# Optimization experiments

Hardware: AMD Instinct MI355X
Metric: run time of the kernel (lower is better)

## Reference

```python
import jax, jax.numpy as jnp
import numpy as np

HIDDEN = 2048
HEADS = 16
HEAD_DIM = HIDDEN // HEADS          # 128
HALF = HEAD_DIM // 2                # 64
LATENT = HIDDEN // 4                # 512 (compression_ratio=4)
ROPE_BASE = 10000.0


def _rope_cos_sin(seq_len):
    # LlamaRotaryEmbedding with dim=HALF
    inv_freq = 1.0 / (ROPE_BASE ** (jnp.arange(0, HALF, 2, dtype=jnp.float32) / HALF))
    t = jnp.arange(seq_len, dtype=jnp.float32)
    freqs = jnp.einsum('i,j->ij', t, inv_freq)          # [S, HALF/2]
    emb = jnp.concatenate([freqs, freqs], axis=-1)       # [S, HALF]
    cos = jnp.cos(emb)[None, :, None, :]                 # [1,S,1,HALF]
    sin = jnp.sin(emb)[None, :, None, :]
    return cos, sin


def _rotate_half(x):
    x1, x2 = jnp.split(x, 2, axis=-1)
    return jnp.concatenate([-x2, x1], axis=-1)


def _apply_rope(x, cos, sin):
    return x * cos + _rotate_half(x) * sin


def setup_inputs() -> dict:
    key = jax.random.key(0)
    ks = jax.random.split(key, 10)
    B, S = 2, 2048
    std = 0.02
    inp = {
        'x':        jax.random.normal(ks[0], (B, S, HIDDEN), jnp.float32),
        # weights stored as [in, out] (transposed torch Linear weight)
        'W_kv_d':   jax.random.normal(ks[1], (HIDDEN, LATENT), jnp.float32) * std,
        'W_q_d':    jax.random.normal(ks[2], (HIDDEN, LATENT), jnp.float32) * std,
        'W_k_u':    jax.random.normal(ks[3], (LATENT, HEADS * HALF), jnp.float32) * std,
        'W_q_u':    jax.random.normal(ks[4], (LATENT, HEADS * HALF), jnp.float32) * std,
        'W_v_u':    jax.random.normal(ks[5], (LATENT, HIDDEN), jnp.float32) * std,
        'W_rope_k': jax.random.normal(ks[6], (HIDDEN, HIDDEN // 2), jnp.float32) * std,
        'W_rope_q': jax.random.normal(ks[7], (LATENT, HIDDEN // 2), jnp.float32) * std,
        'W_o':      jax.random.normal(ks[8], (HIDDEN, HIDDEN), jnp.float32) * std,
    }
    return inp


def reference(x, W_kv_d, W_q_d, W_k_u, W_q_u, W_v_u, W_rope_k, W_rope_q, W_o):
    B, S, _ = x.shape
    kv_latent = x @ W_kv_d                      # [B,S,LATENT]
    q_latent = x @ W_q_d                        # [B,S,LATENT]

    k = (kv_latent @ W_k_u).reshape(B, S, HEADS, HALF)
    q = (q_latent @ W_q_u).reshape(B, S, HEADS, HALF)
    v = (kv_latent @ W_v_u).reshape(B, S, HEADS, HEAD_DIM)

    q_rope = (q_latent @ W_rope_q).reshape(B, S, HEADS, HALF)
    k_rope = (x @ W_rope_k).reshape(B, S, HEADS, HALF)

    cos, sin = _rope_cos_sin(S)
    k_rope = _apply_rope(k_rope, cos, sin)
    q_rope = _apply_rope(q_rope, cos, sin)

    q = jnp.concatenate([q, q_rope], axis=-1)   # [B,S,H,HEAD_DIM]
    k = jnp.concatenate([k, k_rope], axis=-1)

    scale = 1.0 / jnp.sqrt(jnp.float32(HEAD_DIM))
    scores = jnp.einsum('bqhd,bkhd->bhqk', q, k) * scale   # [B,H,S,S]
    causal = jnp.tril(jnp.ones((S, S), dtype=bool))
    scores = jnp.where(causal[None, None], scores, jnp.float32(-1e30))
    attn = jax.nn.softmax(scores, axis=-1)
    y = jnp.einsum('bhqk,bkhd->bqhd', attn, v).reshape(B, S, HIDDEN)
    return y @ W_o
```

## Files before the change

### kernel.cpp

```cpp
#include <hip/hip_runtime.h>
#include <hip/hip_bf16.h>

typedef __hip_bfloat16 bf16;
typedef __attribute__((ext_vector_type(8))) short short8;
typedef __attribute__((ext_vector_type(4))) float f32x4;

#define AS1 __attribute__((address_space(1)))
#define AS3 __attribute__((address_space(3)))

__device__ __forceinline__ void gload_lds16(const bf16* gp, bf16* lp) {
  __builtin_amdgcn_global_load_lds((const AS1 void*)gp, (AS3 void*)lp, 16, 0, 0);
}

__device__ __forceinline__ float fast_exp2(float x) {
#if __has_builtin(__builtin_amdgcn_exp2f)
  return __builtin_amdgcn_exp2f(x);
#else
  return exp2f(x);
#endif
}

__device__ __forceinline__ void store_c(bf16* C, size_t idx, float v) { C[idx] = __float2bfloat16(v); }
__device__ __forceinline__ void store_c(float* C, size_t idx, float v) { C[idx] = v; }

struct __align__(8) b16x4 { bf16 a, b, c, d; };

__global__ void cvt_f32_bf16(const float* __restrict__ in, bf16* __restrict__ out) {
  const int i = (blockIdx.x * 256 + threadIdx.x) * 4;
  const float4 v = *(const float4*)(in + i);
  out[i + 0] = __float2bfloat16(v.x);
  out[i + 1] = __float2bfloat16(v.y);
  out[i + 2] = __float2bfloat16(v.z);
  out[i + 3] = __float2bfloat16(v.w);
}

__global__ void rope_tab_kernel(float2* __restrict__ ctab) {
  const int idx = blockIdx.x * 256 + threadIdx.x;
  const int i = idx & 31;
  const int s = idx >> 5;
  const float inv = fast_exp2(-(float)i * 0.41524101186092029f);
  const float ang = (float)s * inv;
  ctab[idx] = make_float2(cosf(ang), sinf(ang));
}

struct PrepArgs {
  const float* src[8];
  bf16* dst[8];
  int R[8], C[8], cum[8];
};

__global__ void prep_kernel(PrepArgs a) {
  __shared__ bf16 t[32][33];
  const int blk = blockIdx.x;
  int e = 0;
  while (e < 7 && blk >= a.cum[e]) ++e;
  const int lt = blk - (e ? a.cum[e - 1] : 0);
  const int R = a.R[e], C = a.C[e];
  const int tpr = C >> 5;
  const int bx = lt % tpr, by = lt / tpr;
  const float* in = a.src[e];
  bf16* out = a.dst[e];
  const int c0 = bx * 32, r0 = by * 32;
  const int tx = threadIdx.x, ty = threadIdx.y;
  for (int i = 0; i < 4; ++i)
    t[ty + 8 * i][tx] = __float2bfloat16(in[(size_t)(r0 + ty + 8 * i) * C + c0 + tx]);
  __syncthreads();
  for (int i = 0; i < 4; ++i)
    out[(size_t)(c0 + ty + 8 * i) * R + r0 + tx] = t[tx][ty + 8 * i];
}

template <typename CT, int MODE>
__global__ void gemm_bt(const bf16* __restrict__ A, int lda,
                        const bf16* __restrict__ Bt,
                        CT* __restrict__ C, bf16* __restrict__ C2, int ldc,
                        int K, const float2* __restrict__ ctab)
{
  __shared__ __align__(16) bf16 As[2][128 * 32];
  __shared__ __align__(16) bf16 Bs[2][128 * 32];
  const int tid  = threadIdx.x;
  const int wave = tid >> 6, lane = tid & 63;
  const int quad = lane >> 4, l16 = lane & 15;
  const int m0 = blockIdx.y * 128, n0 = blockIdx.x * 128;
  const int wm = (wave >> 1) * 64, wn = (wave & 1) * 64;

  f32x4 acc[4][4];
#pragma unroll
  for (int i = 0; i < 4; ++i)
#pragma unroll
    for (int j = 0; j < 4; ++j) acc[i][j] = (f32x4){0.f, 0.f, 0.f, 0.f};

  const int r1  = tid >> 2;
  const int ks1 = (tid & 3) * 8;

  gload_lds16(A  + (size_t)(m0 + r1)      * lda + ks1, &As[0][tid * 8]);
  gload_lds16(A  + (size_t)(m0 + r1 + 64) * lda + ks1, &As[0][(tid + 256) * 8]);
  gload_lds16(Bt + (size_t)(n0 + r1)      * K   + ks1, &Bs[0][tid * 8]);
  gload_lds16(Bt + (size_t)(n0 + r1 + 64) * K   + ks1, &Bs[0][(tid + 256) * 8]);

  int cur = 0;
  for (int k0 = 0; k0 < K; k0 += 32) {
    if (k0 + 32 < K) {
      const int kn = k0 + 32;
      const int nxt = cur ^ 1;
      gload_lds16(A  + (size_t)(m0 + r1)      * lda + kn + ks1, &As[nxt][tid * 8]);
      gload_lds16(A  + (size_t)(m0 + r1 + 64) * lda + kn + ks1, &As[nxt][(tid + 256) * 8]);
      gload_lds16(Bt + (size_t)(n0 + r1)      * K   + kn + ks1, &Bs[nxt][tid * 8]);
      gload_lds16(Bt + (size_t)(n0 + r1 + 64) * K   + kn + ks1, &Bs[nxt][(tid + 256) * 8]);
      asm volatile("s_waitcnt vmcnt(4)" ::: "memory");
    } else {
      asm volatile("s_waitcnt vmcnt(0)" ::: "memory");
    }
    __builtin_amdgcn_s_barrier();

    short8 af[4], bf_[4];
#pragma unroll
    for (int mt = 0; mt < 4; ++mt)
      af[mt] = *(const short8*)&As[cur][(wm + mt * 16 + l16) * 32 + quad * 8];
#pragma unroll
    for (int nt = 0; nt < 4; ++nt)
      bf_[nt] = *(const short8*)&Bs[cur][(wn + nt * 16 + l16) * 32 + quad * 8];
#pragma unroll
    for (int mt = 0; mt < 4; ++mt)
#pragma unroll
      for (int nt = 0; nt < 4; ++nt)
        acc[mt][nt] = __builtin_amdgcn_mfma_f32_16x16x32_bf16(af[mt], bf_[nt], acc[mt][nt], 0, 0, 0);
    __builtin_amdgcn_s_barrier();
    cur ^= 1;
  }

  if (MODE == 0) {
#pragma unroll
    for (int mt = 0; mt < 4; ++mt) {
      const int row = m0 + wm + mt * 16 + quad * 4;
#pragma unroll
      for (int nt = 0; nt < 4; ++nt) {
        const int cn = n0 + wn + nt * 16 + l16;
        const f32x4 v = acc[mt][nt];
#pragma unroll
        for (int r = 0; r < 4; ++r)
          store_c(C, (size_t)(row + r) * ldc + cn, v[r]);
      }
    }
  } else if (MODE == 4) {
    if (n0 < 1024) {
#pragma unroll
      for (int mt = 0; mt < 4; ++mt) {
        const int row = m0 + wm + mt * 16 + quad * 4;
#pragma unroll
        for (int nt = 0; nt < 4; ++nt) {
          const int cn = n0 + wn + nt * 16 + l16;
          const f32x4 v = acc[mt][nt];
#pragma unroll
          for (int r = 0; r < 4; ++r)
            store_c(C, (size_t)(row + r) * 1024 + cn, v[r]);
        }
      }
    } else {
#pragma unroll
      for (int mt = 0; mt < 4; ++mt) {
        const int row = m0 + wm + mt * 16 + quad * 4;
        f32x4 w[4];
#pragma unroll
        for (int nt = 0; nt < 4; ++nt) w[nt] = acc[mt][nt];
#pragma unroll
        for (int r = 0; r < 4; ++r) {
          const int s = (row + r) & 2047;
          const float2 cs0 = ctab[(s << 5) + l16];
          const float2 cs1 = ctab[(s << 5) + 16 + l16];
          const float x1a = w[0][r], x2a = w[2][r];
          const float x1b = w[1][r], x2b = w[3][r];
          w[0][r] = x1a * cs0.x - x2a * cs0.y;
          w[2][r] = x2a * cs0.x + x1a * cs0.y;
          w[1][r] = x1b * cs1.x - x2b * cs1.y;
          w[3][r] = x2b * cs1.x + x1b * cs1.y;
        }
#pragma unroll
        for (int nt = 0; nt < 4; ++nt) {
          const int cn2 = n0 + wn + nt * 16 + l16 - 1024;
          const int g = ((cn2 >> 6) << 7) + 64 + (cn2 & 63);
#pragma unroll
          for (int r = 0; r < 4; ++r)
            C2[(size_t)(row + r) * 2048 + g] = __float2bfloat16(w[nt][r]);
        }
      }
    }
  }
}

__global__ void gemm_up_fused(const bf16* __restrict__ latcat,
                              const bf16* __restrict__ wtUP,
                              const bf16* __restrict__ wtQcat,
                              bf16* __restrict__ vT, bf16* __restrict__ kfull,
                              bf16* __restrict__ qfull,
                              const float2* __restrict__ ctab)
{
  const bool is2 = (blockIdx.x >= 24);
  const bf16* A  = latcat + (is2 ? 512 : 0);
  const bf16* Bt = is2 ? wtQcat : wtUP;
  const int n0 = (is2 ? (int)blockIdx.x - 24 : (int)blockIdx.x) * 128;
  const int K = 512, lda = 1024;

  __shared__ __align__(16) bf16 As[2][128 * 32];
  __shared__ __align__(16) bf16 Bs[2][128 * 32];
  const int tid  = threadIdx.x;
  const int wave = tid >> 6, lane = tid & 63;
  const int quad = lane >> 4, l16 = lane & 15;
  const int m0 = blockIdx.y * 128;
  const int wm = (wave >> 1) * 64, wn = (wave & 1) * 64;

  f32x4 acc[4][4];
#pragma unroll
  for (int i = 0; i < 4; ++i)
#pragma unroll
    for (int j = 0; j < 4; ++j) acc[i][j] = (f32x4){0.f, 0.f, 0.f, 0.f};

  const int r1  = tid >> 2;
  const int ks1 = (tid & 3) * 8;

  gload_lds16(A  + (size_t)(m0 + r1)      * lda + ks1, &As[0][tid * 8]);
  gload_lds16(A  + (size_t)(m0 + r1 + 64) * lda + ks1, &As[0][(tid + 256) * 8]);
  gload_lds16(Bt + (size_t)(n0 + r1)      * K   + ks1, &Bs[0][tid * 8]);
  gload_lds16(Bt + (size_t)(n0 + r1 + 64) * K   + ks1, &Bs[0][(tid + 256) * 8]);

  int cur = 0;
  for (int k0 = 0; k0 < K; k0 += 32) {
    if (k0 + 32 < K) {
      const int kn = k0 + 32;
      const int nxt = cur ^ 1;
      gload_lds16(A  + (size_t)(m0 + r1)      * lda + kn + ks1, &As[nxt][tid * 8]);
      gload_lds16(A  + (size_t)(m0 + r1 + 64) * lda + kn + ks1, &As[nxt][(tid + 256) * 8]);
      gload_lds16(Bt + (size_t)(n0 + r1)      * K   + kn + ks1, &Bs[nxt][tid * 8]);
      gload_lds16(Bt + (size_t)(n0 + r1 + 64) * K   + kn + ks1, &Bs[nxt][(tid + 256) * 8]);
      asm volatile("s_waitcnt vmcnt(4)" ::: "memory");
    } else {
      asm volatile("s_waitcnt vmcnt(0)" ::: "memory");
    }
    __builtin_amdgcn_s_barrier();

    short8 af[4], bf_[4];
#pragma unroll
    for (int mt = 0; mt < 4; ++mt)
      af[mt] = *(const short8*)&As[cur][(wm + mt * 16 + l16) * 32 + quad * 8];
#pragma unroll
    for (int nt = 0; nt < 4; ++nt)
      bf_[nt] = *(const short8*)&Bs[cur][(wn + nt * 16 + l16) * 32 + quad * 8];
#pragma unroll
    for (int mt = 0; mt < 4; ++mt)
#pragma unroll
      for (int nt = 0; nt < 4; ++nt)
        acc[mt][nt] = __builtin_amdgcn_mfma_f32_16x16x32_bf16(af[mt], bf_[nt], acc[mt][nt], 0, 0, 0);
    __builtin_amdgcn_s_barrier();
    cur ^= 1;
  }

  if (is2) {
    if (n0 < 1024) {
#pragma unroll
      for (int mt = 0; mt < 4; ++mt) {
        const int row = m0 + wm + mt * 16 + quad * 4;
#pragma unroll
        for (int nt = 0; nt < 4; ++nt) {
          const int cn = n0 + wn + nt * 16 + l16;
          const int g = (((cn >> 6) & 15) << 7) + ((cn >> 10) << 6) + (cn & 63);
          const f32x4 v = acc[mt][nt];
#pragma unroll
          for (int r = 0; r < 4; ++r)
            qfull[(size_t)(row + r) * 2048 + g] = __float2bfloat16(v[r]);
        }
      }
    } else {
#pragma unroll
      for (int mt = 0; mt < 4; ++mt) {
        const int row = m0 + wm + mt * 16 + quad * 4;
        f32x4 w[4];
#pragma unroll
        for (int nt = 0; nt < 4; ++nt) w[nt] = acc[mt][nt];
#pragma unroll
        for (int r = 0; r < 4; ++r) {
          const int s = (row + r) & 2047;
          const float2 cs0 = ctab[(s << 5) + l16];
          const float2 cs1 = ctab[(s << 5) + 16 + l16];
          const float x1a = w[0][r], x2a = w[2][r];
          const float x1b = w[1][r], x2b = w[3][r];
          w[0][r] = x1a * cs0.x - x2a * cs0.y;
          w[2][r] = x2a * cs0.x + x1a * cs0.y;
          w[1][r] = x1b * cs1.x - x2b * cs1.y;
          w[3][r] = x2b * cs1.x + x1b * cs1.y;
        }
#pragma unroll
        for (int nt = 0; nt < 4; ++nt) {
          const int cn = n0 + wn + nt * 16 + l16;
          const int g = (((cn >> 6) & 15) << 7) + ((cn >> 10) << 6) + (cn & 63);
#pragma unroll
          for (int r = 0; r < 4; ++r)
            qfull[(size_t)(row + r) * 2048 + g] = __float2bfloat16(w[nt][r]);
        }
      }
    }
  } else {
#pragma unroll
    for (int mt = 0; mt < 4; ++mt) {
      const int row = m0 + wm + mt * 16 + quad * 4;
#pragma unroll
      for (int nt = 0; nt < 4; ++nt) {
        const int cn = n0 + wn + nt * 16 + l16;
        const f32x4 v = acc[mt][nt];
        if (cn < 1024) {
          const int g = ((cn >> 6) << 7) + (cn & 63);
#pragma unroll
          for (int r = 0; r < 4; ++r)
            kfull[(size_t)(row + r) * 2048 + g] = __float2bfloat16(v[r]);
        } else {
          const int cn2 = cn - 1024;
          const int bb = row >> 11, s0 = row & 2047;
          b16x4 pk;
          pk.a = __float2bfloat16(v[0]); pk.b = __float2bfloat16(v[1]);
          pk.c = __float2bfloat16(v[2]); pk.d = __float2bfloat16(v[3]);
          *(b16x4*)(vT + ((size_t)(bb * 2048 + cn2)) * 2048 + s0) = pk;
        }
      }
    }
  }
}

__global__ __launch_bounds__(256, 2) void attn7_kernel(
    const bf16* __restrict__ Q, const bf16* __restrict__ Kf,
    const bf16* __restrict__ VT, bf16* __restrict__ Y)
{
  __shared__ __align__(16) bf16 Ks[64 * 128];
  __shared__ __align__(16) bf16 VTs[128 * 64];
  __shared__ __align__(16) bf16 Ps[4 * 32 * 64];
  const int tid  = threadIdx.x;
  const int wave = tid >> 6, lane = tid & 63;
  const int quad = lane >> 4, l16 = lane & 15;
  const int bh = blockIdx.x;
  const int yy = blockIdx.y;
  const int aa = yy & 7;
  const int qt = (yy >> 3) ? (15 - aa) : aa;
  const size_t kqbase = ((size_t)(bh >> 4) * 2048) * 2048 + (bh & 15) * 128;
  const size_t vtbase = (size_t)bh * 128 * 2048;
  const float C2 = 0.08838834764831845f * 1.4426950408889634f;
  const float MNEG = -30.0f;

  short8 ones;
#pragma unroll
  for (int i = 0; i < 8; ++i) ones[i] = (short)0x3F80;

  const int krow = tid >> 4, kcol = (tid & 15) * 8;
  const int vrow = tid >> 3, vcol = (tid & 7) * 8;

  const int q0 = qt * 128;
  const int T = 2 * qt + 2;
  const int wq0 = q0 + wave * 32;
  const int psbase = wave * (32 * 64);

  short8 qf[2][4];
#pragma unroll
  for (int m = 0; m < 2; ++m) {
    const bf16* qp = Q + kqbase + (size_t)(wq0 + m * 16 + l16) * 2048 + quad * 8;
#pragma unroll
    for (int kc = 0; kc < 4; ++kc) qf[m][kc] = *(const short8*)(qp + kc * 32);
  }
  f32x4 o[2][8];
#pragma unroll
  for (int m = 0; m < 2; ++m)
#pragma unroll
    for (int i = 0; i < 8; ++i) o[m][i] = (f32x4){0, 0, 0, 0};
  f32x4 lacc[2];
  lacc[0] = (f32x4){0, 0, 0, 0};
  lacc[1] = (f32x4){0, 0, 0, 0};

  short8 kg[4], vg[4];
#pragma unroll
  for (int i = 0; i < 4; ++i)
    kg[i] = *(const short8*)(Kf + kqbase + (size_t)(krow + i * 16) * 2048 + kcol);
#pragma unroll
  for (int i = 0; i < 4; ++i)
    vg[i] = *(const short8*)(VT + vtbase + (size_t)(vrow + i * 32) * 2048 + vcol);

  for (int t = 0; t < T; ++t) {
    const int k0 = t * 64;
    __syncthreads();
#pragma unroll
    for (int i = 0; i < 4; ++i) {
      const int rw = krow + i * 16;
      *(short8*)&Ks[rw * 128 + (kcol ^ ((rw & 7) * 8))] = kg[i];
    }
#pragma unroll
    for (int i = 0; i < 4; ++i) {
      const int rw = vrow + i * 32;
      *(short8*)&VTs[rw * 64 + (vcol ^ ((rw & 7) * 8))] = vg[i];
    }
    __syncthreads();
    if (t + 1 < T) {
      const int kn = k0 + 64;
#pragma unroll
      for (int i = 0; i < 4; ++i)
        kg[i] = *(const short8*)(Kf + kqbase + (size_t)(kn + krow + i * 16) * 2048 + kcol);
#pragma unroll
      for (int i = 0; i < 4; ++i)
        vg[i] = *(const short8*)(VT + vtbase + (size_t)(vrow + i * 32) * 2048 + kn + vcol);
    }

    if (k0 <= wq0 + 31) {
      f32x4 sf[2][4];
#pragma unroll
      for (int m = 0; m < 2; ++m)
#pragma unroll
        for (int kt = 0; kt < 4; ++kt) sf[m][kt] = (f32x4){0, 0, 0, 0};
#pragma unroll
      for (int kt = 0; kt < 4; ++kt) {
#pragma unroll
        for (int kc = 0; kc < 4; ++kc) {
          const short8 bfr = *(const short8*)&Ks[(kt * 16 + l16) * 128 +
                                                ((kc * 32 + quad * 8) ^ ((l16 & 7) * 8))];
          sf[0][kt] = __builtin_amdgcn_mfma_f32_16x16x32_bf16(qf[0][kc], bfr, sf[0][kt], 0, 0, 0);
          sf[1][kt] = __builtin_amdgcn_mfma_f32_16x16x32_bf16(qf[1][kc], bfr, sf[1][kt], 0, 0, 0);
        }
      }
#pragma unroll
      for (int m = 0; m < 2; ++m) {
        const int row0m = wq0 + m * 16 + quad * 4;
        if (k0 + 63 > row0m) {
#pragma unroll
          for (int kt = 0; kt < 4; ++kt) {
            const int col = k0 + kt * 16 + l16;
#pragma unroll
            for (int r = 0; r < 4; ++r)
              sf[m][kt][r] = (col > row0m + r) ? -3e38f : sf[m][kt][r];
          }
        }
      }
#pragma unroll
      for (int m = 0; m < 2; ++m)
#pragma unroll
        for (int kt = 0; kt < 4; ++kt)
#pragma unroll
          for (int r = 0; r < 4; ++r) {
            const float p = fast_exp2(__builtin_fmaf(sf[m][kt][r], C2, MNEG));
            const int prow = m * 16 + quad * 4 + r;
            const int pcol = (kt * 16 + l16) ^ (quad * 16);
            Ps[psbase + prow * 64 + pcol] = __float2bfloat16(p);
          }
      asm volatile("s_waitcnt lgkmcnt(0)" ::: "memory");
#pragma unroll
      for (int kc = 0; kc < 2; ++kc) {
        short8 ap[2];
#pragma unroll
        for (int m = 0; m < 2; ++m) {
          const int acol = (kc * 32 + quad * 8) ^ (((l16 >> 2) & 3) * 16);
          ap[m] = *(const short8*)&Ps[psbase + (m * 16 + l16) * 64 + acol];
          lacc[m] = __builtin_amdgcn_mfma_f32_16x16x32_bf16(ap[m], ones, lacc[m], 0, 0, 0);
        }
#pragma unroll
        for (int dt = 0; dt < 8; ++dt) {
          const short8 vb = *(const short8*)&VTs[(dt * 16 + l16) * 64 +
                                                ((kc * 32 + quad * 8) ^ ((l16 & 7) * 8))];
          o[0][dt] = __builtin_amdgcn_mfma_f32_16x16x32_bf16(ap[0], vb, o[0][dt], 0, 0, 0);
          o[1][dt] = __builtin_amdgcn_mfma_f32_16x16x32_bf16(ap[1], vb, o[1][dt], 0, 0, 0);
        }
      }
    }
  }

#pragma unroll
  for (int m = 0; m < 2; ++m) {
    const int row0m = wq0 + m * 16 + quad * 4;
#pragma unroll
    for (int r = 0; r < 4; ++r) {
      const float inv = 1.0f / lacc[m][r];
#pragma unroll
      for (int dt = 0; dt < 8; ++dt)
        Y[kqbase + (size_t)(row0m + r) * 2048 + dt * 16 + l16] =
            __float2bfloat16(o[m][dt][r] * inv);
    }
  }
}

extern "C" void kernel_launch(void* const* d_in, const int* in_sizes, int n_in,
                              void* d_out, int out_size, void* d_ws, size_t ws_size,
                              hipStream_t stream)
{
  const float* x      = (const float*)d_in[0];
  const float* Wkvd   = (const float*)d_in[1];
  const float* Wqd    = (const float*)d_in[2];
  const float* Wku    = (const float*)d_in[3];
  const float* Wqu    = (const float*)d_in[4];
  const float* Wvu    = (const float*)d_in[5];
  const float* Wropek = (const float*)d_in[6];
  const float* Wropeq = (const float*)d_in[7];
  const float* Wo     = (const float*)d_in[8];

  char* ws = (char*)d_ws;
  size_t off = 0;
  auto alloc = [&](size_t elems) {
    bf16* p = (bf16*)(ws + off);
    off += ((elems * sizeof(bf16) + 255) & ~(size_t)255);
    return p;
  };
  bf16* wtX    = alloc((size_t)2048 * 2048);
  bf16* wtUP   = alloc((size_t)3072 * 512);
  bf16* wtQcat = alloc((size_t)2048 * 512);
  bf16* latcat = alloc((size_t)4096 * 1024);
  bf16* wt_o   = alloc((size_t)2048 * 2048);
  bf16* xbf    = alloc((size_t)4096 * 2048);
  bf16* qfull  = alloc((size_t)4096 * 2048);
  bf16* kfull  = alloc((size_t)4096 * 2048);
  float2* ctab = (float2*)alloc((size_t)65536 * 4);
  bf16* ybuf   = (bf16*)ws;
  bf16* vT     = (bf16*)d_out;
  (void)ws_size; (void)in_sizes; (void)n_in; (void)out_size;

  rope_tab_kernel<<<256, 256, 0, stream>>>(ctab);
  cvt_f32_bf16<<<8192, 256, 0, stream>>>(x, xbf);

  PrepArgs pa;
  const float* srcs[8] = {Wkvd, Wqd, Wropek, Wku, Wvu, Wqu, Wropeq, Wo};
  bf16* dsts[8] = {wtX, wtX + (size_t)512 * 2048, wtX + (size_t)1024 * 2048,
                   wtUP, wtUP + (size_t)1024 * 512,
                   wtQcat, wtQcat + (size_t)1024 * 512, wt_o};
  const int Rs[8] = {2048, 2048, 2048, 512, 512, 512, 512, 2048};
  const int Cs[8] = {512, 512, 1024, 1024, 2048, 1024, 1024, 2048};
  int cum = 0;
  for (int e = 0; e < 8; ++e) {
    pa.src[e] = srcs[e]; pa.dst[e] = dsts[e]; pa.R[e] = Rs[e]; pa.C[e] = Cs[e];
    cum += (Rs[e] >> 5) * (Cs[e] >> 5);
    pa.cum[e] = cum;
  }
  prep_kernel<<<cum, dim3(32, 8), 0, stream>>>(pa);

  gemm_bt<bf16, 4><<<dim3(16, 32), 256, 0, stream>>>(xbf, 2048, wtX, latcat, kfull, 1024, 2048, ctab);
  gemm_up_fused<<<dim3(40, 32), 256, 0, stream>>>(latcat, wtUP, wtQcat, vT, kfull, qfull, ctab);

  attn7_kernel<<<dim3(32, 16), 256, 0, stream>>>(qfull, kfull, vT, ybuf);
  gemm_bt<float, 0><<<dim3(16, 32), 256, 0, stream>>>(ybuf, 2048, wt_o, (float*)d_out, (bf16*)nullptr, 2048, 2048, ctab);
}
```

Before: 324.1 us.

## Balance causal attention by splitting key ranges across paired q-tiles with merge

Each attention block now processes a fixed amount of key tiles: the high q-tile's tail keys and the low q-tile's full range, storing unnormalized partial outputs and row sums. A new merge kernel adds the two partial results per row and normalizes. This removes the load imbalance between blocks handling early vs late causal tiles, at the cost of an extra kernel, extra global traffic for partials, and bf16 rounding of unnormalized partials.

```diff
diff --git a/kernel.cpp b/kernel.cpp
--- a/kernel.cpp
+++ b/kernel.cpp
@@ -323,9 +323,126 @@
   }
 }
 
-__global__ __launch_bounds__(256, 2) void attn7_kernel(
+__device__ __forceinline__ void attn_phase(
     const bf16* __restrict__ Q, const bf16* __restrict__ Kf,
-    const bf16* __restrict__ VT, bf16* __restrict__ Y)
+    const bf16* __restrict__ VT,
+    size_t kqbase, size_t vtbase, int qt, int t0, int t1,
+    bf16* __restrict__ Ks, bf16* __restrict__ VTs, bf16* __restrict__ Psw,
+    f32x4 (&o)[2][8], f32x4 (&lacc)[2], const short8 ones,
+    int wave, int quad, int l16, int krow, int kcol, int vrow, int vcol)
+{
+  const float C2 = 0.08838834764831845f * 1.4426950408889634f;
+  const float MNEG = -30.0f;
+  const int wq0 = qt * 128 + wave * 32;
+
+  short8 qf[2][4];
+#pragma unroll
+  for (int m = 0; m < 2; ++m) {
+    const bf16* qp = Q + kqbase + (size_t)(wq0 + m * 16 + l16) * 2048 + quad * 8;
+#pragma unroll
+    for (int kc = 0; kc < 4; ++kc) qf[m][kc] = *(const short8*)(qp + kc * 32);
+  }
+
+  short8 kg[4], vg[4];
+  {
+    const int kk = t0 * 64;
+#pragma unroll
+    for (int i = 0; i < 4; ++i)
+      kg[i] = *(const short8*)(Kf + kqbase + (size_t)(kk + krow + i * 16) * 2048 + kcol);
+#pragma unroll
+    for (int i = 0; i < 4; ++i)
+      vg[i] = *(const short8*)(VT + vtbase + (size_t)(vrow + i * 32) * 2048 + kk + vcol);
+  }
+
+  for (int t = t0; t < t1; ++t) {
+    const int k0 = t * 64;
+    __syncthreads();
+#pragma unroll
+    for (int i = 0; i < 4; ++i) {
+      const int rw = krow + i * 16;
+      *(short8*)&Ks[rw * 128 + (kcol ^ ((rw & 7) * 8))] = kg[i];
+    }
+#pragma unroll
+    for (int i = 0; i < 4; ++i) {
+      const int rw = vrow + i * 32;
+      *(short8*)&VTs[rw * 64 + (vcol ^ ((rw & 7) * 8))] = vg[i];
+    }
+    __syncthreads();
+    if (t + 1 < t1) {
+      const int kn = k0 + 64;
+#pragma unroll
+      for (int i = 0; i < 4; ++i)
+        kg[i] = *(const short8*)(Kf + kqbase + (size_t)(kn + krow + i * 16) * 2048 + kcol);
+#pragma unroll
+      for (int i = 0; i < 4; ++i)
+        vg[i] = *(const short8*)(VT + vtbase + (size_t)(vrow + i * 32) * 2048 + kn + vcol);
+    }
+    if (k0 > wq0 + 31) continue;
+
+    f32x4 sf[2][4];
+#pragma unroll
+    for (int kt = 0; kt < 4; ++kt) {
+      sf[0][kt] = (f32x4){0, 0, 0, 0};
+      sf[1][kt] = (f32x4){0, 0, 0, 0};
+    }
+#pragma unroll
+    for (int kt = 0; kt < 4; ++kt) {
+#pragma unroll
+      for (int kc = 0; kc < 4; ++kc) {
+        const short8 bfr = *(const short8*)&Ks[(kt * 16 + l16) * 128 +
+                                              ((kc * 32 + quad * 8) ^ ((l16 & 7) * 8))];
+        sf[0][kt] = __builtin_amdgcn_mfma_f32_16x16x32_bf16(qf[0][kc], bfr, sf[0][kt], 0, 0, 0);
+        sf[1][kt] = __builtin_amdgcn_mfma_f32_16x16x32_bf16(qf[1][kc], bfr, sf[1][kt], 0, 0, 0);
+      }
+    }
+#pragma unroll
+    for (int m = 0; m < 2; ++m) {
+      const int row0m = wq0 + m * 16 + quad * 4;
+      if (k0 + 63 > row0m) {
+#pragma unroll
+        for (int kt = 0; kt < 4; ++kt) {
+          const int col = k0 + kt * 16 + l16;
+#pragma unroll
+          for (int r = 0; r < 4; ++r)
+            sf[m][kt][r] = (col > row0m + r) ? -3e38f : sf[m][kt][r];
+        }
+      }
+    }
+#pragma unroll
+    for (int m = 0; m < 2; ++m)
+#pragma unroll
+      for (int kt = 0; kt < 4; ++kt)
+#pragma unroll
+        for (int r = 0; r < 4; ++r) {
+          const float p = fast_exp2(__builtin_fmaf(sf[m][kt][r], C2, MNEG));
+          const int prow = m * 16 + quad * 4 + r;
+          const int pcol = (kt * 16 + l16) ^ (quad * 16);
+          Psw[prow * 64 + pcol] = __float2bfloat16(p);
+        }
+    asm volatile("s_waitcnt lgkmcnt(0)" ::: "memory");
+#pragma unroll
+    for (int kc = 0; kc < 2; ++kc) {
+      short8 ap[2];
+      const int acol = (kc * 32 + quad * 8) ^ (((l16 >> 2) & 3) * 16);
+      ap[0] = *(const short8*)&Psw[l16 * 64 + acol];
+      lacc[0] = __builtin_amdgcn_mfma_f32_16x16x32_bf16(ap[0], ones, lacc[0], 0, 0, 0);
+      ap[1] = *(const short8*)&Psw[(16 + l16) * 64 + acol];
+      lacc[1] = __builtin_amdgcn_mfma_f32_16x16x32_bf16(ap[1], ones, lacc[1], 0, 0, 0);
+#pragma unroll
+      for (int dt = 0; dt < 8; ++dt) {
+        const short8 vb = *(const short8*)&VTs[(dt * 16 + l16) * 64 +
+                                              ((kc * 32 + quad * 8) ^ ((l16 & 7) * 8))];
+        o[0][dt] = __builtin_amdgcn_mfma_f32_16x16x32_bf16(ap[0], vb, o[0][dt], 0, 0, 0);
+        o[1][dt] = __builtin_amdgcn_mfma_f32_16x16x32_bf16(ap[1], vb, o[1][dt], 0, 0, 0);
+      }
+    }
+  }
+}
+
+__global__ __launch_bounds__(256, 2) void attn10_kernel(
+    const bf16* __restrict__ Q, const bf16* __restrict__ Kf,
+    const bf16* __restrict__ VT, bf16* __restrict__ Y,
+    bf16* __restrict__ poA, float* __restrict__ lA, float* __restrict__ lB)
 {
   __shared__ __align__(16) bf16 Ks[64 * 128];
   __shared__ __align__(16) bf16 VTs[128 * 64];
@@ -334,13 +451,11 @@
   const int wave = tid >> 6, lane = tid & 63;
   const int quad = lane >> 4, l16 = lane & 15;
   const int bh = blockIdx.x;
-  const int yy = blockIdx.y;
-  const int aa = yy & 7;
-  const int qt = (yy >> 3) ? (15 - aa) : aa;
+  const int j  = blockIdx.y;
+  const int qt_A = 15 - j;
+  const int qt_B = j;
   const size_t kqbase = ((size_t)(bh >> 4) * 2048) * 2048 + (bh & 15) * 128;
   const size_t vtbase = (size_t)bh * 128 * 2048;
-  const float C2 = 0.08838834764831845f * 1.4426950408889634f;
-  const float MNEG = -30.0f;
 
   short8 ones;
 #pragma unroll
@@ -348,133 +463,80 @@
 
   const int krow = tid >> 4, kcol = (tid & 15) * 8;
   const int vrow = tid >> 3, vcol = (tid & 7) * 8;
-
-  const int q0 = qt * 128;
-  const int T = 2 * qt + 2;
-  const int wq0 = q0 + wave * 32;
-  const int psbase = wave * (32 * 64);
-
-  short8 qf[2][4];
-#pragma unroll
-  for (int m = 0; m < 2; ++m) {
-    const bf16* qp = Q + kqbase + (size_t)(wq0 + m * 16 + l16) * 2048 + quad * 8;
-#pragma unroll
-    for (int kc = 0; kc < 4; ++kc) qf[m][kc] = *(const short8*)(qp + kc * 32);
-  }
+  bf16* Psw = Ps + wave * (32 * 64);
+
   f32x4 o[2][8];
+  f32x4 lacc[2];
+
 #pragma unroll
   for (int m = 0; m < 2; ++m)
 #pragma unroll
     for (int i = 0; i < 8; ++i) o[m][i] = (f32x4){0, 0, 0, 0};
-  f32x4 lacc[2];
   lacc[0] = (f32x4){0, 0, 0, 0};
   lacc[1] = (f32x4){0, 0, 0, 0};
-
-  short8 kg[4], vg[4];
-#pragma unroll
-  for (int i = 0; i < 4; ++i)
-    kg[i] = *(const short8*)(Kf + kqbase + (size_t)(krow + i * 16) * 2048 + kcol);
-#pragma unroll
-  for (int i = 0; i < 4; ++i)
-    vg[i] = *(const short8*)(VT + vtbase + (size_t)(vrow + i * 32) * 2048 + vcol);
-
-  for (int t = 0; t < T; ++t) {
-    const int k0 = t * 64;
-    __syncthreads();
-#pragma unroll
-    for (int i = 0; i < 4; ++i) {
-      const int rw = krow + i * 16;
-      *(short8*)&Ks[rw * 128 + (kcol ^ ((rw & 7) * 8))] = kg[i];
-    }
-#pragma unroll
-    for (int i = 0; i < 4; ++i) {
-      const int rw = vrow + i * 32;
-      *(short8*)&VTs[rw * 64 + (vcol ^ ((rw & 7) * 8))] = vg[i];
-    }
-    __syncthreads();
-    if (t + 1 < T) {
-      const int kn = k0 + 64;
-#pragma unroll
-      for (int i = 0; i < 4; ++i)
-        kg[i] = *(const short8*)(Kf + kqbase + (size_t)(kn + krow + i * 16) * 2048 + kcol);
-#pragma unroll
-      for (int i = 0; i < 4; ++i)
-        vg[i] = *(const short8*)(VT + vtbase + (size_t)(vrow + i * 32) * 2048 + kn + vcol);
-    }
-
-    if (k0 <= wq0 + 31) {
-      f32x4 sf[2][4];
-#pragma unroll
-      for (int m = 0; m < 2; ++m)
-#pragma unroll
-        for (int kt = 0; kt < 4; ++kt) sf[m][kt] = (f32x4){0, 0, 0, 0};
-#pragma unroll
-      for (int kt = 0; kt < 4; ++kt) {
-#pragma unroll
-        for (int kc = 0; kc < 4; ++kc) {
-          const short8 bfr = *(const short8*)&Ks[(kt * 16 + l16) * 128 +
-                                                ((kc * 32 + quad * 8) ^ ((l16 & 7) * 8))];
-          sf[0][kt] = __builtin_amdgcn_mfma_f32_16x16x32_bf16(qf[0][kc], bfr, sf[0][kt], 0, 0, 0);
-          sf[1][kt] = __builtin_amdgcn_mfma_f32_16x16x32_bf16(qf[1][kc], bfr, sf[1][kt], 0, 0, 0);
-        }
-      }
-#pragma unroll
-      for (int m = 0; m < 2; ++m) {
-        const int row0m = wq0 + m * 16 + quad * 4;
-        if (k0 + 63 > row0m) {
-#pragma unroll
-          for (int kt = 0; kt < 4; ++kt) {
-            const int col = k0 + kt * 16 + l16;
-#pragma unroll
-            for (int r = 0; r < 4; ++r)
-              sf[m][kt][r] = (col > row0m + r) ? -3e38f : sf[m][kt][r];
-          }
-        }
-      }
-#pragma unroll
-      for (int m = 0; m < 2; ++m)
-#pragma unroll
-        for (int kt = 0; kt < 4; ++kt)
-#pragma unroll
-          for (int r = 0; r < 4; ++r) {
-            const float p = fast_exp2(__builtin_fmaf(sf[m][kt][r], C2, MNEG));
-            const int prow = m * 16 + quad * 4 + r;
-            const int pcol = (kt * 16 + l16) ^ (quad * 16);
-            Ps[psbase + prow * 64 + pcol] = __float2bfloat16(p);
-          }
-      asm volatile("s_waitcnt lgkmcnt(0)" ::: "memory");
-#pragma unroll
-      for (int kc = 0; kc < 2; ++kc) {
-        short8 ap[2];
-#pragma unroll
-        for (int m = 0; m < 2; ++m) {
-          const int acol = (kc * 32 + quad * 8) ^ (((l16 >> 2) & 3) * 16);
-          ap[m] = *(const short8*)&Ps[psbase + (m * 16 + l16) * 64 + acol];
-          lacc[m] = __builtin_amdgcn_mfma_f32_16x16x32_bf16(ap[m], ones, lacc[m], 0, 0, 0);
-        }
-#pragma unroll
-        for (int dt = 0; dt < 8; ++dt) {
-          const short8 vb = *(const short8*)&VTs[(dt * 16 + l16) * 64 +
-                                                ((kc * 32 + quad * 8) ^ ((l16 & 7) * 8))];
-          o[0][dt] = __builtin_amdgcn_mfma_f32_16x16x32_bf16(ap[0], vb, o[0][dt], 0, 0, 0);
-          o[1][dt] = __builtin_amdgcn_mfma_f32_16x16x32_bf16(ap[1], vb, o[1][dt], 0, 0, 0);
-        }
-      }
-    }
-  }
-
-#pragma unroll
-  for (int m = 0; m < 2; ++m) {
-    const int row0m = wq0 + m * 16 + quad * 4;
-#pragma unroll
-    for (int r = 0; r < 4; ++r) {
-      const float inv = 1.0f / lacc[m][r];
-#pragma unroll
-      for (int dt = 0; dt < 8; ++dt)
-        Y[kqbase + (size_t)(row0m + r) * 2048 + dt * 16 + l16] =
-            __float2bfloat16(o[m][dt][r] * inv);
-    }
-  }
+  attn_phase(Q, Kf, VT, kqbase, vtbase, qt_A, qt_A + 1, 2 * qt_A + 2,
+             Ks, VTs, Psw, o, lacc, ones, wave, quad, l16, krow, kcol, vrow, vcol);
+  {
+    bf16* po = poA + ((size_t)(bh * 16 + qt_A) << 14);
+    float* pl = lA + ((bh * 16 + qt_A) << 7);
+#pragma unroll
+    for (int m = 0; m < 2; ++m)
+#pragma unroll
+      for (int r = 0; r < 4; ++r) {
+        const int rl = wave * 32 + m * 16 + quad * 4 + r;
+#pragma unroll
+        for (int dt = 0; dt < 8; ++dt)
+          po[rl * 128 + dt * 16 + l16] = __float2bfloat16(o[m][dt][r]);
+        if (l16 == 0) pl[rl] = lacc[m][r];
+      }
+  }
+
+#pragma unroll
+  for (int m = 0; m < 2; ++m)
+#pragma unroll
+    for (int i = 0; i < 8; ++i) o[m][i] = (f32x4){0, 0, 0, 0};
+  lacc[0] = (f32x4){0, 0, 0, 0};
+  lacc[1] = (f32x4){0, 0, 0, 0};
+  attn_phase(Q, Kf, VT, kqbase, vtbase, qt_B, 0, qt_B + 1,
+             Ks, VTs, Psw, o, lacc, ones, wave, quad, l16, krow, kcol, vrow, vcol);
+  {
+    float* pl = lB + ((bh * 16 + qt_B) << 7);
+#pragma unroll
+    for (int m = 0; m < 2; ++m)
+#pragma unroll
+      for (int r = 0; r < 4; ++r) {
+        const int rl = wave * 32 + m * 16 + quad * 4 + r;
+#pragma unroll
+        for (int dt = 0; dt < 8; ++dt)
+          Y[kqbase + (size_t)(qt_B * 128 + rl) * 2048 + dt * 16 + l16] =
+              __float2bfloat16(o[m][dt][r]);
+        if (l16 == 0) pl[rl] = lacc[m][r];
+      }
+  }
+}
+
+__global__ void attn_merge(bf16* __restrict__ Y, const bf16* __restrict__ poA,
+                           const float* __restrict__ lA, const float* __restrict__ lB)
+{
+  const int t = blockIdx.x * 256 + threadIdx.x;
+  const size_t e = (size_t)t * 8;
+  const int col = (int)(e & 2047);
+  const int row = (int)(e >> 11);
+  const int b = row >> 11, s = row & 2047;
+  const int h = col >> 7, dcol = col & 127;
+  const int bh = b * 16 + h, qt = s >> 7, rl = s & 127;
+  const int li = ((bh * 16 + qt) << 7) + rl;
+  const float inv = 1.0f / (lA[li] + lB[li]);
+  const short8 va = *(const short8*)(poA + (((size_t)(bh * 16 + qt)) << 14) + rl * 128 + dcol);
+  const short8 vb = *(const short8*)(Y + e);
+  short8 out;
+#pragma unroll
+  for (int i = 0; i < 8; ++i) {
+    const float fa = __bfloat162float(((const bf16*)&va)[i]);
+    const float fb = __bfloat162float(((const bf16*)&vb)[i]);
+    ((bf16*)&out)[i] = __float2bfloat16((fa + fb) * inv);
+  }
+  *(short8*)(Y + e) = out;
 }
 
 extern "C" void kernel_launch(void* const* d_in, const int* in_sizes, int n_in,
@@ -509,6 +571,9 @@
   float2* ctab = (float2*)alloc((size_t)65536 * 4);
   bf16* ybuf   = (bf16*)ws;
   bf16* vT     = (bf16*)d_out;
+  bf16*  poA = xbf;
+  float* lA  = (float*)(ws + 16777216);
+  float* lB  = (float*)(ws + 16777216 + 262144);
   (void)ws_size; (void)in_sizes; (void)n_in; (void)out_size;
 
   rope_tab_kernel<<<256, 256, 0, stream>>>(ctab);
@@ -532,6 +597,7 @@
   gemm_bt<bf16, 4><<<dim3(16, 32), 256, 0, stream>>>(xbf, 2048, wtX, latcat, kfull, 1024, 2048, ctab);
   gemm_up_fused<<<dim3(40, 32), 256, 0, stream>>>(latcat, wtUP, wtQcat, vT, kfull, qfull, ctab);
 
-  attn7_kernel<<<dim3(32, 16), 256, 0, stream>>>(qfull, kfull, vT, ybuf);
+  attn10_kernel<<<dim3(32, 16), 256, 0, stream>>>(qfull, kfull, vT, ybuf, poA, lA, lB);
+  attn_merge<<<4096, 256, 0, stream>>>(ybuf, poA, lA, lB);
   gemm_bt<float, 0><<<dim3(16, 32), 256, 0, stream>>>(ybuf, 2048, wt_o, (float*)d_out, (bf16*)nullptr, 2048, 2048, ctab);
 }
```

Measured after the change: 325.0 us. About the same (+0.3%).
